# Kernel tuning notes

Measured on AMD Instinct MI355X. Metric: run time of the kernel, lower is better.

## Reference

```python
import jax, jax.numpy as jnp
import numpy as np

N = 100000      # nodes
E = 3200000     # edges (avg degree 32)
G = 64          # graphs in batch
IN_C = 128      # in_channels
HID = 16        # hidden_channels
OUT_C = 8       # out_channels
EDGE_C = 16     # edge_channels


def setup_inputs() -> dict:
    key = jax.random.key(0)
    ks = jax.random.split(key, 10)
    x = jax.random.normal(ks[0], (N, IN_C), dtype=jnp.float32)
    edge_index = jax.random.randint(ks[1], (2, E), 0, N, dtype=jnp.int64)
    edge_attr = jax.random.normal(ks[2], (E, EDGE_C), dtype=jnp.float32)
    batch_index = jnp.sort(jax.random.randint(ks[3], (N,), 0, G, dtype=jnp.int64))
    def lin(k, fan_in, fan_out):
        bound = 1.0 / np.sqrt(fan_in)
        return jax.random.uniform(k, (fan_in, fan_out), jnp.float32, -bound, bound)
    return {
        "x": x,
        "edge_index": edge_index,
        "edge_attr": edge_attr,
        "batch_index": batch_index,
        "W1_node": lin(ks[4], IN_C, HID),
        "W1_edge": lin(ks[5], EDGE_C, HID),
        "W2_node": lin(ks[6], HID, HID),
        "W2_edge": lin(ks[7], EDGE_C, HID),
        "node_W": lin(ks[8], HID, OUT_C),
        "node_b": jax.random.uniform(ks[9], (OUT_C,), jnp.float32, -1.0 / np.sqrt(HID), 1.0 / np.sqrt(HID)),
    }


def _gcn_conv(h, edge_attr_pad, src, dst, norm, W_node, W_edge, n_nodes):
    # node/edge linear transforms (no bias, as in lin_node/lin_edge)
    node_emb = h @ W_node                       # [N, H]
    edge_emb = edge_attr_pad @ W_edge           # [E+N, H]
    # message: norm * (x_j + edge_attr), scatter-add at destination
    msg = norm[:, None] * (node_emb[src] + edge_emb)
    return jax.ops.segment_sum(msg, dst, num_segments=n_nodes)


def reference(x, edge_index, edge_attr, batch_index,
              W1_node, W1_edge, W2_node, W2_edge, node_W, node_b):
    n = x.shape[0]
    loop = jnp.arange(n, dtype=edge_index.dtype)
    src = jnp.concatenate([edge_index[0], loop])          # add_self_loops
    dst = jnp.concatenate([edge_index[1], loop])
    ea = jnp.concatenate(
        [edge_attr, jnp.zeros((n, edge_attr.shape[1]), edge_attr.dtype)], axis=0)
    # symmetric gcn_norm: deg from target index, norm = d^-1/2[src]*d^-1/2[dst]
    deg = jax.ops.segment_sum(jnp.ones_like(src, dtype=x.dtype), dst, num_segments=n)
    dinv = jnp.where(deg > 0, jax.lax.rsqrt(jnp.maximum(deg, 1.0)), 0.0)
    norm = dinv[src] * dinv[dst]

    h = jax.nn.relu(_gcn_conv(x, ea, src, dst, norm, W1_node, W1_edge, n))
    h = jax.nn.relu(_gcn_conv(h, ea, src, dst, norm, W2_node, W2_edge, n))

    # global mean pool over graphs
    ones = jnp.ones((n,), x.dtype)
    counts = jax.ops.segment_sum(ones, batch_index, num_segments=G)
    pooled = jax.ops.segment_sum(h, batch_index, num_segments=G)
    pooled = pooled / jnp.maximum(counts, 1.0)[:, None]

    return pooled @ node_W + node_b
```

## Files before the change

### kernel.cpp

```cpp
#include <hip/hip_runtime.h>
#include <hip/hip_bf16.h>

#define IN_C   128
#define HID    16
#define OUT_C  8
#define EDGE_C 16
#define NG     64
#define NRANGE 8

__global__ void deg_kernel(const int* __restrict__ dst, int* __restrict__ deg, int E) {
    int e = blockIdx.x * blockDim.x + threadIdx.x;
    if (e < E) atomicAdd(&deg[dst[e]], 1);
}

__global__ void scanA_kernel(const int* __restrict__ deg, int* __restrict__ row_start,
                             int* __restrict__ blocksum, int n) {
    __shared__ int s[256];
    int t = threadIdx.x;
    int i = blockIdx.x * 256 + t;
    int own = (i < n) ? deg[i] : 0;
    s[t] = own; __syncthreads();
    for (int off = 1; off < 256; off <<= 1) {
        int v = (t >= off) ? s[t - off] : 0;
        __syncthreads();
        s[t] += v;
        __syncthreads();
    }
    if (i < n) row_start[i] = s[t] - own;
    if (t == 255) blocksum[blockIdx.x] = s[255];
}

__global__ void scanB_kernel(int* __restrict__ blocksum, int nb) {
    __shared__ int s[512];
    int t = threadIdx.x;
    int own = (t < nb) ? blocksum[t] : 0;
    s[t] = own; __syncthreads();
    for (int off = 1; off < 512; off <<= 1) {
        int v = (t >= off) ? s[t - off] : 0;
        __syncthreads();
        s[t] += v;
        __syncthreads();
    }
    if (t < nb) blocksum[t] = s[t] - own;
}

__global__ void scanC_kernel(const int* __restrict__ deg, int* __restrict__ row_start,
                             const int* __restrict__ blocksum,
                             int* __restrict__ cursor, float* __restrict__ dinv, int n) {
    int i = blockIdx.x * 256 + threadIdx.x;
    if (i < n) {
        int rs = row_start[i] + blocksum[blockIdx.x];
        row_start[i] = rs;
        cursor[i] = rs;
        dinv[i] = rsqrtf((float)deg[i] + 1.0f);
    }
}

__global__ void fill_kernel(const int* __restrict__ src, const int* __restrict__ dst,
                            int* __restrict__ cursor, int2* __restrict__ adj,
                            int E, int range_size, int bpr) {
    int r = blockIdx.x & (NRANGE - 1);
    int q = blockIdx.x >> 3;
    int lo = r * range_size;
    int hi = lo + range_size;
    long long chunk = ((long long)E + bpr - 1) / bpr;
    int e0 = (int)((long long)q * chunk);
    long long e1l = (long long)e0 + chunk;
    int e1 = (e1l < E) ? (int)e1l : E;
#pragma unroll 4
    for (int e = e0 + threadIdx.x; e < e1; e += blockDim.x) {
        int d = __builtin_nontemporal_load(dst + e);
        if (d >= lo && d < hi) {
            int s = __builtin_nontemporal_load(src + e);
            int pos = atomicAdd(&cursor[d], 1);
            adj[pos] = make_int2(e, s);
        }
    }
}

__global__ void xform1_kernel(const float* __restrict__ x, const float* __restrict__ W,
                              const float* __restrict__ dinv, float* __restrict__ a1, int n) {
    int t = threadIdx.x;
    int v = blockIdx.x * 16 + (t >> 4);
    int c = t & 15;
    if (v >= n) return;
    const float4* xr = (const float4*)(x + (size_t)v * IN_C);
    float acc = 0.0f;
#pragma unroll
    for (int k4 = 0; k4 < IN_C / 4; ++k4) {
        float4 xv = xr[k4];
        int k = k4 * 4;
        acc += xv.x * W[(k + 0) * HID + c];
        acc += xv.y * W[(k + 1) * HID + c];
        acc += xv.z * W[(k + 2) * HID + c];
        acc += xv.w * W[(k + 3) * HID + c];
    }
    a1[(size_t)v * HID + c] = dinv[v] * acc;
}

__global__ void gather1_kernel(const int2* __restrict__ adj, const int* __restrict__ row_start,
                               const int* __restrict__ deg,
                               const float* __restrict__ edge_attr,
                               const float* __restrict__ W1e, const float* __restrict__ W2n,
                               const float* __restrict__ a1, const float* __restrict__ dinv,
                               float* __restrict__ a2, float* __restrict__ ES, int n) {
    int t = threadIdx.x;
    int lane = t & 63;
    int slot = lane >> 4;
    int c = lane & 15;
    float we[EDGE_C], wn[HID];
#pragma unroll
    for (int k = 0; k < EDGE_C; ++k) we[k] = W1e[k * HID + c];
#pragma unroll
    for (int k = 0; k < HID; ++k) wn[k] = W2n[k * HID + c];
    int v = blockIdx.x * 4 + (t >> 6);
    if (v >= n) return;
    int start = row_start[v];
    int dg = deg[v];
    float es = 0.0f, s1 = 0.0f;
    for (int base = 0; base < dg; base += 64) {
        int m = dg - base; if (m > 64) m = 64;
        int e_my = 0, s_my = 0;
        float ds_my = 0.0f;
        if (lane < m) {
            long long adv = __builtin_nontemporal_load(
                (const long long*)&adj[start + base + lane]);
            e_my = (int)(adv & 0xffffffffLL);
            s_my = (int)(adv >> 32);
            ds_my = dinv[s_my];
        }
#pragma unroll 4
        for (int i = slot; i < m; i += 4) {
            int e = __shfl(e_my, i, 64);
            int s = __shfl(s_my, i, 64);
            float ds = __shfl(ds_my, i, 64);
            es += ds * __builtin_nontemporal_load(edge_attr + (size_t)e * EDGE_C + c);
            s1 += a1[s * HID + c];
        }
    }
    es += __shfl_xor(es, 16, 64); es += __shfl_xor(es, 32, 64);
    s1 += __shfl_xor(s1, 16, 64); s1 += __shfl_xor(s1, 32, 64);
    float dv = dinv[v];
    int lanebase = lane & ~15;
    float e1 = 0.0f;
#pragma unroll
    for (int k = 0; k < EDGE_C; ++k)
        e1 += __shfl(es, lanebase + k, 64) * we[k];
    float h = fmaxf(dv * (s1 + a1[(size_t)v * HID + c] + e1), 0.0f);
    float o = 0.0f;
#pragma unroll
    for (int k = 0; k < HID; ++k)
        o += __shfl(h, lanebase + k, 64) * wn[k];
    if (slot == 0) {
        a2[(size_t)v * HID + c] = dv * o;
        ES[(size_t)v * HID + c] = es;
    }
}

__global__ void gather2_kernel(const int2* __restrict__ adj, const int* __restrict__ row_start,
                               const int* __restrict__ deg,
                               const float* __restrict__ W2e,
                               const float* __restrict__ a2, const float* __restrict__ dinv,
                               const float* __restrict__ ES, float* __restrict__ h2, int n) {
    int t = threadIdx.x;
    int lane = t & 63;
    int slot = lane >> 4;
    int c = lane & 15;
    float we[EDGE_C];
#pragma unroll
    for (int k = 0; k < EDGE_C; ++k) we[k] = W2e[k * HID + c];
    int v = blockIdx.x * 4 + (t >> 6);
    if (v >= n) return;
    int start = row_start[v];
    int dg = deg[v];
    float s2 = 0.0f;
    for (int base = 0; base < dg; base += 64) {
        int m = dg - base; if (m > 64) m = 64;
        int s_my = 0;
        if (lane < m) {
            long long adv = __builtin_nontemporal_load(
                (const long long*)&adj[start + base + lane]);
            s_my = (int)(adv >> 32);
        }
#pragma unroll 4
        for (int i = slot; i < m; i += 4) {
            int s = __shfl(s_my, i, 64);
            s2 += a2[s * HID + c];
        }
    }
    s2 += __shfl_xor(s2, 16, 64); s2 += __shfl_xor(s2, 32, 64);
    float dv = dinv[v];
    int lanebase = lane & ~15;
    float esv = ES[(size_t)v * HID + c];
    float e2 = 0.0f;
#pragma unroll
    for (int k = 0; k < EDGE_C; ++k)
        e2 += __shfl(esv, lanebase + k, 64) * we[k];
    float h = fmaxf(dv * (s2 + a2[(size_t)v * HID + c] + e2), 0.0f);
    if (slot == 0) h2[(size_t)v * HID + c] = h;
}

__global__ void pool_final_kernel(const float* __restrict__ h2,
                                  const int* __restrict__ batch,
                                  const float* __restrict__ W, const float* __restrict__ b,
                                  float* __restrict__ out, int n) {
    __shared__ float sdata[256];
    int g = blockIdx.x;
    int t = threadIdx.x;
    int c = t & 15;
    int lo = 0, hi = n;
    while (lo < hi) { int m = (lo + hi) >> 1; if (batch[m] < g) lo = m + 1; else hi = m; }
    int start = lo;
    hi = n;
    while (lo < hi) { int m = (lo + hi) >> 1; if (batch[m] < g + 1) lo = m + 1; else hi = m; }
    int end = lo;
    float acc = 0.0f;
    for (int v = start + (t >> 4); v < end; v += 16)
        acc += h2[(size_t)v * HID + c];
    sdata[t] = acc; __syncthreads();
    for (int s = 128; s >= 16; s >>= 1) {
        if (t < s) sdata[t] += sdata[t + s];
        __syncthreads();
    }
    if (t < OUT_C) {
        float inv = 1.0f / fmaxf((float)(end - start), 1.0f);
        float o = b[t];
#pragma unroll
        for (int cc = 0; cc < HID; ++cc)
            o += sdata[cc] * inv * W[cc * OUT_C + t];
        out[g * OUT_C + t] = o;
    }
}

extern "C" void kernel_launch(void* const* d_in, const int* in_sizes, int n_in,
                              void* d_out, int out_size, void* d_ws, size_t ws_size,
                              hipStream_t stream) {
    const float* x         = (const float*)d_in[0];
    const int*   edge_idx  = (const int*)d_in[1];
    const float* edge_attr = (const float*)d_in[2];
    const int*   batch     = (const int*)d_in[3];
    const float* W1_node   = (const float*)d_in[4];
    const float* W1_edge   = (const float*)d_in[5];
    const float* W2_node   = (const float*)d_in[6];
    const float* W2_edge   = (const float*)d_in[7];
    const float* node_W    = (const float*)d_in[8];
    const float* node_b    = (const float*)d_in[9];
    float* out = (float*)d_out;

    const int N = in_sizes[0] / IN_C;
    const int E = in_sizes[1] / 2;
    const int* src = edge_idx;
    const int* dst = edge_idx + E;

    char* p = (char*)d_ws;
    int2*  adj       = (int2*)p;   p += sizeof(int2) * (size_t)E;
    int*   deg       = (int*)p;    p += sizeof(int) * (size_t)N;
    int*   row_start = (int*)p;    p += sizeof(int) * (size_t)N;
    int*   cursor    = (int*)p;    p += sizeof(int) * (size_t)N;
    int*   blocksum  = (int*)p;    p += sizeof(int) * 512;
    float* dinv      = (float*)p;  p += sizeof(float) * (size_t)N;
    float* a1        = (float*)p;  p += sizeof(float) * (size_t)HID * N;
    float* a2        = (float*)p;  p += sizeof(float) * (size_t)HID * N;
    float* ES        = (float*)p;  p += sizeof(float) * (size_t)HID * N;
    float* h2        = a1;

    hipMemsetAsync(deg, 0, sizeof(int) * (size_t)N, stream);

    const int tb = 256;
    const int nbN = (N + 255) / 256;
    deg_kernel <<<(E + tb - 1) / tb, tb, 0, stream>>>(dst, deg, E);
    scanA_kernel<<<nbN, 256, 0, stream>>>(deg, row_start, blocksum, N);
    scanB_kernel<<<1, 512, 0, stream>>>(blocksum, nbN);
    scanC_kernel<<<nbN, 256, 0, stream>>>(deg, row_start, blocksum, cursor, dinv, N);

    const int range_size = (N + NRANGE - 1) / NRANGE;
    const int bpr = 256;
    fill_kernel<<<NRANGE * bpr, tb, 0, stream>>>(src, dst, cursor, adj, E, range_size, bpr);

    xform1_kernel<<<(N + 15) / 16, tb, 0, stream>>>(x, W1_node, dinv, a1, N);

    gather1_kernel<<<(N + 3) / 4, tb, 0, stream>>>(
        adj, row_start, deg, edge_attr, W1_edge, W2_node, a1, dinv, a2, ES, N);
    gather2_kernel<<<(N + 3) / 4, tb, 0, stream>>>(
        adj, row_start, deg, W2_edge, a2, dinv, ES, h2, N);

    pool_final_kernel<<<NG, 256, 0, stream>>>(h2, batch, node_W, node_b, out, N);
}
```

Baseline: 855.8 us.

## Build CSR with two-level bucket binning plus in-LDS per-bucket scatter

Replaces the per-node atomic cursor fill with a two-pass build. The first pass bins edges into 128-node buckets using one atomic counter per bucket and packs the local destination index into the high bits of src. The second pass loads each bucket into shared memory and scatters the edges to their exact CSR positions with LDS atomics. The goal is to make global writes more local and to stop contending on random per-node counters. In exchange, all bucket edges now hit a few hundred hot global counters, the adjacency array gets an extra read/write pass, and any bucket larger than the fixed LDS capacity of 5120 edges is silently truncated.

```diff
diff --git a/kernel.cpp b/kernel.cpp
--- a/kernel.cpp
+++ b/kernel.cpp
@@ -7,6 +7,9 @@
 #define EDGE_C 16
 #define NG     64
 #define NRANGE 8
+#define BSHIFT 7
+#define BNODES 128
+#define LCAP   5120
 
 __global__ void deg_kernel(const int* __restrict__ dst, int* __restrict__ deg, int E) {
     int e = blockIdx.x * blockDim.x + threadIdx.x;
@@ -46,19 +49,17 @@
 
 __global__ void scanC_kernel(const int* __restrict__ deg, int* __restrict__ row_start,
                              const int* __restrict__ blocksum,
-                             int* __restrict__ cursor, float* __restrict__ dinv, int n) {
+                             float* __restrict__ dinv, int n) {
     int i = blockIdx.x * 256 + threadIdx.x;
     if (i < n) {
-        int rs = row_start[i] + blocksum[blockIdx.x];
-        row_start[i] = rs;
-        cursor[i] = rs;
+        row_start[i] = row_start[i] + blocksum[blockIdx.x];
         dinv[i] = rsqrtf((float)deg[i] + 1.0f);
     }
 }
 
-__global__ void fill_kernel(const int* __restrict__ src, const int* __restrict__ dst,
-                            int* __restrict__ cursor, int2* __restrict__ adj,
-                            int E, int range_size, int bpr) {
+__global__ void bin_kernel(const int* __restrict__ src, const int* __restrict__ dst,
+                           const int* __restrict__ row_start, int* __restrict__ bcur,
+                           int2* __restrict__ adj, int E, int range_size, int bpr) {
     int r = blockIdx.x & (NRANGE - 1);
     int q = blockIdx.x >> 3;
     int lo = r * range_size;
@@ -72,9 +73,41 @@
         int d = __builtin_nontemporal_load(dst + e);
         if (d >= lo && d < hi) {
             int s = __builtin_nontemporal_load(src + e);
-            int pos = atomicAdd(&cursor[d], 1);
-            adj[pos] = make_int2(e, s);
-        }
+            int b = d >> BSHIFT;
+            int base = row_start[d & ~(BNODES - 1)];
+            int pos = base + atomicAdd(&bcur[b], 1);
+            adj[pos] = make_int2(e, s | ((d & (BNODES - 1)) << 25));
+        }
+    }
+}
+
+__global__ void csr_kernel(int2* __restrict__ adj, const int* __restrict__ row_start,
+                           int n, int E) {
+    __shared__ int2 buf[LCAP];
+    __shared__ int  rs[BNODES + 1];
+    __shared__ int  cnt[BNODES];
+    int b = blockIdx.x;
+    int lo = b << BSHIFT;
+    int t = threadIdx.x;
+    for (int i = t; i < BNODES + 1; i += 256) {
+        int node = lo + i;
+        rs[i] = (node < n) ? row_start[node] : E;
+    }
+    for (int i = t; i < BNODES; i += 256) cnt[i] = 0;
+    __syncthreads();
+    int base = rs[0];
+    int span = lo + BNODES;
+    int end  = (span <= n) ? rs[BNODES] : rs[n - lo];
+    int L = end - base;
+    if (L > LCAP) L = LCAP;
+    for (int i = t; i < L; i += 256) buf[i] = adj[base + i];
+    __syncthreads();
+    for (int i = t; i < L; i += 256) {
+        int2 v = buf[i];
+        int dl = ((unsigned)v.y) >> 25;
+        int s  = v.y & ((1 << 25) - 1);
+        int pos = rs[dl] + atomicAdd(&cnt[dl], 1);
+        adj[pos] = make_int2(v.x, s);
     }
 }
 
@@ -255,8 +288,8 @@
     char* p = (char*)d_ws;
     int2*  adj       = (int2*)p;   p += sizeof(int2) * (size_t)E;
     int*   deg       = (int*)p;    p += sizeof(int) * (size_t)N;
+    int*   bcur      = (int*)p;    p += sizeof(int) * 1024;
     int*   row_start = (int*)p;    p += sizeof(int) * (size_t)N;
-    int*   cursor    = (int*)p;    p += sizeof(int) * (size_t)N;
     int*   blocksum  = (int*)p;    p += sizeof(int) * 512;
     float* dinv      = (float*)p;  p += sizeof(float) * (size_t)N;
     float* a1        = (float*)p;  p += sizeof(float) * (size_t)HID * N;
@@ -264,18 +297,20 @@
     float* ES        = (float*)p;  p += sizeof(float) * (size_t)HID * N;
     float* h2        = a1;
 
-    hipMemsetAsync(deg, 0, sizeof(int) * (size_t)N, stream);
+    hipMemsetAsync(deg, 0, sizeof(int) * ((size_t)N + 1024), stream);
 
     const int tb = 256;
     const int nbN = (N + 255) / 256;
     deg_kernel <<<(E + tb - 1) / tb, tb, 0, stream>>>(dst, deg, E);
     scanA_kernel<<<nbN, 256, 0, stream>>>(deg, row_start, blocksum, N);
     scanB_kernel<<<1, 512, 0, stream>>>(blocksum, nbN);
-    scanC_kernel<<<nbN, 256, 0, stream>>>(deg, row_start, blocksum, cursor, dinv, N);
+    scanC_kernel<<<nbN, 256, 0, stream>>>(deg, row_start, blocksum, dinv, N);
 
     const int range_size = (N + NRANGE - 1) / NRANGE;
     const int bpr = 256;
-    fill_kernel<<<NRANGE * bpr, tb, 0, stream>>>(src, dst, cursor, adj, E, range_size, bpr);
+    bin_kernel<<<NRANGE * bpr, tb, 0, stream>>>(src, dst, row_start, bcur, adj, E, range_size, bpr);
+    const int nbuck = (N + BNODES - 1) >> BSHIFT;
+    csr_kernel<<<nbuck, 256, 0, stream>>>(adj, row_start, N, E);
 
     xform1_kernel<<<(N + 15) / 16, tb, 0, stream>>>(x, W1_node, dinv, a1, N);
 
```

After: 1.760 ms. 106% more time.
